# Kernel tuning notes

Measured on AMD Instinct MI355X. Metric: run time of the kernel, lower is better.

The kernel has to match this reference:

```python
import jax, jax.numpy as jnp
import numpy as np

BN_EPS = 1e-5

def gin_layer(x, src, dst, w1, b1, w2, b2, gamma, beta):
    # GINConv with eps=0: h_i = MLP(x_i + sum_{j->i} x_j)
    agg = jax.ops.segment_sum(x[src], dst, num_segments=x.shape[0])  # [N, D]
    h = x + agg
    h = jnp.maximum(h @ w1 + b1, 0.0) @ w2 + b2
    # BatchNorm (training-mode batch statistics, biased var as in torch)
    mu = jnp.mean(h, axis=0)
    var = jnp.var(h, axis=0)
    h = (h - mu) * jax.lax.rsqrt(var + BN_EPS) * gamma + beta
    return jnp.maximum(h, 0.0)  # ReLU (dropout = identity in eval)

def setup_inputs() -> dict:
    key = jax.random.key(0)
    N, E, G = 20000, 320000, 64
    dims = [128, 128, 256, 512]
    ks = jax.random.split(key, 32)
    inp = {
        "x": jax.random.normal(ks[0], (N, dims[0]), dtype=jnp.float32),
        "edge_index": jax.random.randint(ks[1], (2, E), 0, N, dtype=jnp.int64),
        "batch_idx": jnp.sort(jax.random.randint(ks[2], (N,), 0, G, dtype=jnp.int64)),
    }
    ki = 3
    for li, (di, do) in enumerate(zip(dims[:-1], dims[1:])):
        s = chr(ord('a') + li)
        inp[f"w1{s}"] = jax.random.normal(ks[ki], (di, do), dtype=jnp.float32) * (1.0 / np.sqrt(di)); ki += 1
        inp[f"b1{s}"] = jnp.zeros((do,), dtype=jnp.float32)
        inp[f"w2{s}"] = jax.random.normal(ks[ki], (do, do), dtype=jnp.float32) * (1.0 / np.sqrt(do)); ki += 1
        inp[f"b2{s}"] = jnp.zeros((do,), dtype=jnp.float32)
        inp[f"gn{s}"] = jnp.ones((do,), dtype=jnp.float32)
        inp[f"bn{s}"] = jnp.zeros((do,), dtype=jnp.float32)
    inp["wo"] = jax.random.normal(ks[ki], (dims[-1], 64), dtype=jnp.float32) * (1.0 / np.sqrt(dims[-1]))
    inp["bo"] = jnp.zeros((64,), dtype=jnp.float32)
    return inp

def reference(x, edge_index, batch_idx,
              w1a, b1a, w2a, b2a, gna, bna,
              w1b, b1b, w2b, b2b, gnb, bnb,
              w1c, b1c, w2c, b2c, gnc, bnc,
              wo, bo):
    G = 64
    src, dst = edge_index[0], edge_index[1]
    h = gin_layer(x, src, dst, w1a, b1a, w2a, b2a, gna, bna)
    h = gin_layer(h, src, dst, w1b, b1b, w2b, b2b, gnb, bnb)
    h = gin_layer(h, src, dst, w1c, b1c, w2c, b2c, gnc, bnc)
    # global mean pool over graphs
    sums = jax.ops.segment_sum(h, batch_idx, num_segments=G)  # [G, 512]
    cnts = jax.ops.segment_sum(jnp.ones((h.shape[0],), h.dtype), batch_idx, num_segments=G)
    pooled = sums / jnp.maximum(cnts, 1.0)[:, None]
    # output projection: Linear -> ReLU (dropout identity in eval)
    return jnp.maximum(pooled @ wo + bo, 0.0)
```

## Files before the change

### kernel.cpp

```cpp
#include <hip/hip_runtime.h>

typedef float f32x4 __attribute__((ext_vector_type(4)));
typedef _Float16 f16x2 __attribute__((ext_vector_type(2)));
typedef _Float16 f16x4 __attribute__((ext_vector_type(4)));
typedef _Float16 f16x8 __attribute__((ext_vector_type(8)));

__device__ __forceinline__ void gload_lds16(const _Float16* g, _Float16* l) {
  __builtin_amdgcn_global_load_lds(
      (const __attribute__((address_space(1))) unsigned int*)g,
      (__attribute__((address_space(3))) unsigned int*)l, 16, 0, 0);
}

__global__ __launch_bounds__(256) void hist_kernel(const int* __restrict__ dst,
                                                   int* __restrict__ deg, int E) {
  int e = blockIdx.x * 256 + threadIdx.x;
  if (e < E) atomicAdd(&deg[dst[e]], 1);
}

__global__ __launch_bounds__(1024) void scan_kernel(const int* __restrict__ deg,
                                                    int* __restrict__ rowstart,
                                                    int* __restrict__ cursor, int N) {
  __shared__ int sums[1024];
  const int t = threadIdx.x;
  const int CH = (N + 1023) >> 10;
  int local[32];
  int base = t * CH;
  int s = 0;
  for (int i = 0; i < CH; i++) {
    int idx = base + i;
    int v = (idx < N) ? deg[idx] : 0;
    local[i] = s;
    s += v;
  }
  sums[t] = s;
  __syncthreads();
  for (int off = 1; off < 1024; off <<= 1) {
    int add = (t >= off) ? sums[t - off] : 0;
    __syncthreads();
    sums[t] += add;
    __syncthreads();
  }
  int prefix = sums[t] - s;
  for (int i = 0; i < CH; i++) {
    int idx = base + i;
    if (idx < N) {
      int v = prefix + local[i];
      rowstart[idx] = v;
      cursor[idx] = v;
    }
  }
  if (t == 1023) rowstart[N] = sums[1023];
}

__global__ __launch_bounds__(256) void fill_kernel(const int* __restrict__ src,
                                                   const int* __restrict__ dst,
                                                   int* __restrict__ cursor,
                                                   int* __restrict__ nbr, int E) {
  int e = blockIdx.x * 256 + threadIdx.x;
  if (e >= E) return;
  int pos = atomicAdd(&cursor[dst[e]], 1);
  nbr[pos] = src[e];
}

__global__ __launch_bounds__(256) void xprep_kernel(const float4* __restrict__ in,
                                                    f16x4* __restrict__ out, int n4,
                                                    int* __restrict__ deg, int N,
                                                    float* __restrict__ zbuf, int zn) {
  int i = blockIdx.x * 256 + threadIdx.x;
  if (i < N) deg[i] = 0;
  if (i < zn) zbuf[i] = 0.f;
  if (i >= n4) return;
  float4 v = in[i];
  f16x4 h;
  h[0] = (_Float16)v.x; h[1] = (_Float16)v.y;
  h[2] = (_Float16)v.z; h[3] = (_Float16)v.w;
  out[i] = h;
}

template <int C, bool BNIN>
__global__ __launch_bounds__(256) void gather_agg_kernel(
    const _Float16* __restrict__ x, const int* __restrict__ rowstart,
    const int* __restrict__ nbr, const float* __restrict__ stats,
    const float* __restrict__ gamma, const float* __restrict__ beta,
    _Float16* __restrict__ agg, int N, float invN) {
  constexpr int Din = 64 * C;
  const int wave = threadIdx.x >> 6;
  const int lane = threadIdx.x & 63;
  const int node = blockIdx.x * 4 + wave;
  if (node >= N) return;

  float sc[C], sh[C];
  if constexpr (BNIN) {
#pragma unroll
    for (int j = 0; j < C; j++) {
      int c = lane * C + j;
      float mean = stats[c] * invN;
      float var = stats[Din + c] * invN - mean * mean;
      sc[j] = rsqrtf(var + 1e-5f) * gamma[c];
      sh[j] = beta[c] - mean * sc[j];
    }
  }

#define LOADROW(dstv, rowidx)                                              \
  {                                                                        \
    const _Float16* _p = x + (size_t)(rowidx)*Din + lane * C;              \
    if constexpr (C == 2) {                                                \
      f16x2 _t = *(const f16x2*)_p;                                        \
      dstv[0] = (float)_t[0]; dstv[1] = (float)_t[1];                      \
    } else {                                                               \
      f16x4 _t = *(const f16x4*)_p;                                        \
      dstv[0] = (float)_t[0]; dstv[1] = (float)_t[1];                      \
      dstv[2] = (float)_t[2]; dstv[3] = (float)_t[3];                      \
    }                                                                      \
  }
#define ACCUM(vv)                                                          \
  _Pragma("unroll") for (int j = 0; j < C; j++)                            \
      acc[j] += BNIN ? fmaxf(vv[j] * sc[j] + sh[j], 0.f) : vv[j];

  float acc[C];
  {
    float v[C];
    LOADROW(v, node)
#pragma unroll
    for (int j = 0; j < C; j++)
      acc[j] = BNIN ? fmaxf(v[j] * sc[j] + sh[j], 0.f) : v[j];
  }
  const int rs = rowstart[node], re = rowstart[node + 1];
  int e = rs;
  for (; e + 3 < re; e += 4) {
    int s0 = nbr[e], s1 = nbr[e + 1], s2 = nbr[e + 2], s3 = nbr[e + 3];
    float v0[C], v1[C], v2[C], v3[C];
    LOADROW(v0, s0)
    LOADROW(v1, s1)
    LOADROW(v2, s2)
    LOADROW(v3, s3)
    ACCUM(v0) ACCUM(v1) ACCUM(v2) ACCUM(v3)
  }
  for (; e + 1 < re; e += 2) {
    int s0 = nbr[e], s1 = nbr[e + 1];
    float v0[C], v1[C];
    LOADROW(v0, s0)
    LOADROW(v1, s1)
    ACCUM(v0) ACCUM(v1)
  }
  if (e < re) {
    int s0 = nbr[e];
    float v0[C];
    LOADROW(v0, s0)
    ACCUM(v0)
  }
#undef ACCUM
#undef LOADROW

  _Float16* o = agg + (size_t)node * Din + lane * C;
  if constexpr (C == 2) {
    f16x2 r; r[0] = (_Float16)acc[0]; r[1] = (_Float16)acc[1];
    *(f16x2*)o = r;
  } else {
    f16x4 r;
    r[0] = (_Float16)acc[0]; r[1] = (_Float16)acc[1];
    r[2] = (_Float16)acc[2]; r[3] = (_Float16)acc[3];
    *(f16x4*)o = r;
  }
}

struct WSeg {
  const float* W;
  _Float16* TH;
  int K, N, total;
};
struct WAll { WSeg s[6]; };

__global__ __launch_bounds__(256) void wprep_all_kernel(WAll a) {
  WSeg sg = a.s[blockIdx.y];
  int idx = blockIdx.x * 256 + threadIdx.x;
  if (idx >= sg.total) return;
  int k = idx / sg.N, n = idx - k * sg.N;
  int KT = sg.K >> 5;
  int frag = (n >> 4) * KT + (k >> 5);
  int slot = (n & 15) | (((k >> 3) & 3) << 4);
  sg.TH[(size_t)frag * 512 + slot * 8 + (k & 7)] = (_Float16)sg.W[idx];
}

template <int RT>
__global__ __launch_bounds__(256, 4) void gemm_mfma_kernel(
    const _Float16* __restrict__ A, const _Float16* __restrict__ BT,
    const float* __restrict__ bias, _Float16* __restrict__ Ch,
    int M, int K, int N, int mblocks, int cbShift,
    int doRelu, float* __restrict__ stats) {
  constexpr int NF = RT / 16;
  constexpr int NFT = 2 * NF;
  constexpr int FPW = NFT / 4;
  __shared__ _Float16 Ah[3][NFT * 512];
  const int bid = blockIdx.x;
  const int xcd = bid & 7;
  const int q = bid >> 3;
  const int r = ((q >> cbShift) << 3) + xcd;
  const int cb = q & ((1 << cbShift) - 1);
  if (r >= mblocks) return;

  const int tid = threadIdx.x;
  const int lane = tid & 63;
  const int w = tid >> 6;
  const int rowBase = r * RT;
  const int colBase = cb * 128 + w * 32;
  const int KT = K >> 5;

  f32x4 acc[NF][2] = {};
  const int c0 = colBase + (lane & 15);
  const size_t bBase0 = ((size_t)(colBase >> 4) * KT) * 512 + (size_t)lane * 8;
  const size_t bBase1 = bBase0 + (size_t)KT * 512;

  size_t srcOff[FPW];
#pragma unroll
  for (int i = 0; i < FPW; i++) {
    int F = w * FPW + i;
    int ks = F / NF, fi = F % NF;
    int row = rowBase + fi * 16 + (lane & 15);
    row = min(row, M - 1);
    srcOff[i] = (size_t)row * K + ks * 32 + ((lane >> 4) << 3);
  }

#define STAGE(b, t)                                                        \
  {                                                                        \
    _Pragma("unroll") for (int i = 0; i < FPW; i++)                        \
        gload_lds16(A + srcOff[i] + (size_t)(t) * 64,                      \
                    &Ah[b][(w * FPW + i) * 512]);                          \
  }

  const int NT = K >> 6;
  STAGE(0, 0)
  if (NT > 1) {
    STAGE(1, 1)
    if constexpr (FPW == 2)
      asm volatile("s_waitcnt vmcnt(2)" ::: "memory");
    else
      asm volatile("s_waitcnt vmcnt(1)" ::: "memory");
  } else {
    asm volatile("s_waitcnt vmcnt(0)" ::: "memory");
  }
  __builtin_amdgcn_s_barrier();
  __builtin_amdgcn_sched_barrier(0);

  int cur = 0;
  for (int t = 0; t < NT; t++) {
    f16x8 bh[2][2];
#pragma unroll
    for (int ks = 0; ks < 2; ks++) {
      int kf = t * 2 + ks;
      bh[ks][0] = *(const f16x8*)(BT + bBase0 + (size_t)kf * 512);
      bh[ks][1] = *(const f16x8*)(BT + bBase1 + (size_t)kf * 512);
    }
    __builtin_amdgcn_sched_barrier(0);
    if (t + 2 < NT) {
      int b2 = (cur >= 1) ? cur - 1 : 2;
      STAGE(b2, t + 2)
    }
    __builtin_amdgcn_sched_barrier(0);
#pragma unroll
    for (int ks = 0; ks < 2; ks++) {
#pragma unroll
      for (int fi = 0; fi < NF; fi++) {
        f16x8 ah = *(const f16x8*)(&Ah[cur][(ks * NF + fi) * 512 + lane * 8]);
        acc[fi][0] = __builtin_amdgcn_mfma_f32_16x16x32_f16(ah, bh[ks][0], acc[fi][0], 0, 0, 0);
        acc[fi][1] = __builtin_amdgcn_mfma_f32_16x16x32_f16(ah, bh[ks][1], acc[fi][1], 0, 0, 0);
      }
    }
    if (t + 1 < NT) {
      __builtin_amdgcn_s_barrier();
      __builtin_amdgcn_sched_barrier(0);
    }
    cur = (cur == 2) ? 0 : cur + 1;
  }
#undef STAGE

  const float bias0 = bias[c0], bias1 = bias[c0 + 16];
  float s1[2] = {0.f, 0.f}, s2[2] = {0.f, 0.f};
  const int rbase = rowBase + (lane >> 4) * 4;
#pragma unroll
  for (int fi = 0; fi < NF; fi++) {
#pragma unroll
    for (int j = 0; j < 4; j++) {
      int row = rbase + fi * 16 + j;
      float v0 = acc[fi][0][j] + bias0;
      float v1 = acc[fi][1][j] + bias1;
      if (doRelu) { v0 = fmaxf(v0, 0.f); v1 = fmaxf(v1, 0.f); }
      if (row < M) {
        Ch[(size_t)row * N + c0] = (_Float16)v0;
        Ch[(size_t)row * N + c0 + 16] = (_Float16)v1;
        s1[0] += v0; s2[0] += v0 * v0;
        s1[1] += v1; s2[1] += v1 * v1;
      }
    }
  }
  if (stats) {
#pragma unroll
    for (int off = 16; off < 64; off <<= 1) {
      s1[0] += __shfl_xor(s1[0], off);
      s2[0] += __shfl_xor(s2[0], off);
      s1[1] += __shfl_xor(s1[1], off);
      s2[1] += __shfl_xor(s2[1], off);
    }
    if (lane < 16) {
      atomicAdd(&stats[c0], s1[0]);
      atomicAdd(&stats[N + c0], s2[0]);
      atomicAdd(&stats[c0 + 16], s1[1]);
      atomicAdd(&stats[N + c0 + 16], s2[1]);
    }
  }
}

__global__ __launch_bounds__(256) void bn_pool_kernel(
    const _Float16* __restrict__ h, const float* __restrict__ stats,
    const float* __restrict__ gamma, const float* __restrict__ beta,
    const int* __restrict__ batch, float* __restrict__ pooled, int N, float invN) {
  const int g = blockIdx.x >> 3;
  const int s = blockIdx.x & 7;
  __shared__ int s_lo, s_hi;
  if (threadIdx.x == 0) {
    int lo = 0, hi = N;
    while (lo < hi) { int m = (lo + hi) >> 1; if (batch[m] < g) lo = m + 1; else hi = m; }
    s_lo = lo;
    lo = 0; hi = N;
    while (lo < hi) { int m = (lo + hi) >> 1; if (batch[m] < g + 1) lo = m + 1; else hi = m; }
    s_hi = lo;
  }
  __syncthreads();
  const int lo = s_lo, hi = s_hi, len = hi - lo;
  if (len == 0) return;
  const int per = (len + 7) >> 3;
  const int rs = lo + s * per;
  const int re = min(rs + per, hi);
  if (rs >= re) return;
  const int t = threadIdx.x;
  float scv[2], shv[2];
#pragma unroll
  for (int j = 0; j < 2; j++) {
    int c = 2 * t + j;
    float mean = stats[c] * invN;
    float var = stats[512 + c] * invN - mean * mean;
    scv[j] = rsqrtf(var + 1e-5f) * gamma[c];
    shv[j] = beta[c] - mean * scv[j];
  }
  float ax = 0.f, ay = 0.f;
  for (int r = rs; r < re; r++) {
    f16x2 v = *(const f16x2*)(h + (size_t)r * 512 + 2 * t);
    ax += fmaxf((float)v[0] * scv[0] + shv[0], 0.f);
    ay += fmaxf((float)v[1] * scv[1] + shv[1], 0.f);
  }
  float inv = 1.f / (float)len;
  atomicAdd(&pooled[g * 512 + 2 * t], ax * inv);
  atomicAdd(&pooled[g * 512 + 2 * t + 1], ay * inv);
}

__global__ __launch_bounds__(64) void out_kernel(const float* __restrict__ pooled,
                                                 const float* __restrict__ wo,
                                                 const float* __restrict__ bo,
                                                 float* __restrict__ out) {
  int g = blockIdx.x, o = threadIdx.x;
  float acc = bo[o];
  for (int c = 0; c < 512; c++) acc += pooled[g * 512 + c] * wo[c * 64 + o];
  out[g * 64 + o] = fmaxf(acc, 0.f);
}

extern "C" void kernel_launch(void* const* d_in, const int* in_sizes, int n_in,
                              void* d_out, int out_size, void* d_ws, size_t ws_size,
                              hipStream_t stream) {
  const float* x0 = (const float*)d_in[0];
  const int* ei = (const int*)d_in[1];
  const int* batch = (const int*)d_in[2];
  const int N = in_sizes[0] / 128;
  const int E = in_sizes[1] / 2;
  const int* src = ei;
  const int* dst = ei + E;
  const float* W[3][6];
  for (int li = 0; li < 3; li++)
    for (int k = 0; k < 6; k++) W[li][k] = (const float*)d_in[3 + li * 6 + k];
  const float* wo = (const float*)d_in[21];
  const float* bo = (const float*)d_in[22];
  float* out = (float*)d_out;

  float* stats3 = (float*)d_ws;
  float* pooled = stats3 + 3 * 1024;
  int* deg = (int*)(pooled + 64 * 512);
  int* rowstart = deg + N;
  int* cursor = rowstart + N + 1;
  int* nbr = cursor + N;
  uintptr_t wp = (uintptr_t)(nbr + E);
  wp = (wp + 15) & ~(uintptr_t)15;
  _Float16* aggh = (_Float16*)wp;
  _Float16* h1h = aggh + (size_t)N * 256;
  _Float16* h2h = h1h + (size_t)N * 512;
  _Float16* x0h = h2h + (size_t)N * 512;
  _Float16* wbuf = x0h + (size_t)N * 128;

  const int dins[3] = {128, 128, 256};
  const int douts[3] = {128, 256, 512};

  _Float16* WT[3][2];
  {
    _Float16* p = wbuf;
    for (int li = 0; li < 3; li++) {
      WT[li][0] = p; p += (size_t)dins[li] * douts[li];
      WT[li][1] = p; p += (size_t)douts[li] * douts[li];
    }
  }
  {
    WAll wa;
    int maxTotal = 0;
    for (int li = 0; li < 3; li++) {
      int e1 = dins[li] * douts[li];
      int e2 = douts[li] * douts[li];
      wa.s[li * 2 + 0] = WSeg{W[li][0], WT[li][0], dins[li], douts[li], e1};
      wa.s[li * 2 + 1] = WSeg{W[li][2], WT[li][1], douts[li], douts[li], e2};
      maxTotal = max(maxTotal, max(e1, e2));
    }
    dim3 g((maxTotal + 255) / 256, 6);
    wprep_all_kernel<<<g, 256, 0, stream>>>(wa);
  }

  {
    int n4 = N * 32;
    int zn = 3 * 1024 + 64 * 512;
    xprep_kernel<<<(n4 + 255) / 256, 256, 0, stream>>>(
        (const float4*)x0, (f16x4*)x0h, n4, deg, N, stats3, zn);
  }

  hist_kernel<<<(E + 255) / 256, 256, 0, stream>>>(dst, deg, E);
  scan_kernel<<<1, 1024, 0, stream>>>(deg, rowstart, cursor, N);
  fill_kernel<<<(E + 255) / 256, 256, 0, stream>>>(src, dst, cursor, nbr, E);

  const int mb64 = (N + 63) / 64;
  const int mb64_8 = ((mb64 + 7) / 8) * 8;
  const int mb32 = (N + 31) / 32;
  const int mb32_8 = ((mb32 + 7) / 8) * 8;
  const int gblocks = (N + 3) / 4;
  const float invN = 1.0f / N;

  for (int li = 0; li < 3; li++) {
    int Din = dins[li], Dout = douts[li];
    float* stats = stats3 + li * 1024;
    if (li == 0)
      gather_agg_kernel<2, false><<<gblocks, 256, 0, stream>>>(
          x0h, rowstart, nbr, nullptr, nullptr, nullptr, aggh, N, invN);
    else if (li == 1)
      gather_agg_kernel<2, true><<<gblocks, 256, 0, stream>>>(
          h2h, rowstart, nbr, stats3 + 0 * 1024, W[0][4], W[0][5], aggh, N, invN);
    else
      gather_agg_kernel<4, true><<<gblocks, 256, 0, stream>>>(
          h2h, rowstart, nbr, stats3 + 1 * 1024, W[1][4], W[1][5], aggh, N, invN);

    if (Dout == 128) {
      gemm_mfma_kernel<32><<<mb32_8, 256, 0, stream>>>(aggh, WT[li][0], W[li][1], h1h,
                                                       N, Din, Dout, mb32, 0, 1, nullptr);
      gemm_mfma_kernel<32><<<mb32_8, 256, 0, stream>>>(h1h, WT[li][1], W[li][3], h2h,
                                                       N, Dout, Dout, mb32, 0, 0, stats);
    } else {
      int cbShift = (Dout == 256) ? 1 : 2;
      int nblocks = mb64_8 << cbShift;
      gemm_mfma_kernel<64><<<nblocks, 256, 0, stream>>>(aggh, WT[li][0], W[li][1], h1h,
                                                        N, Din, Dout, mb64, cbShift, 1, nullptr);
      gemm_mfma_kernel<64><<<nblocks, 256, 0, stream>>>(h1h, WT[li][1], W[li][3], h2h,
                                                        N, Dout, Dout, mb64, cbShift, 0, stats);
    }
    if (li == 2) {
      bn_pool_kernel<<<64 * 8, 256, 0, stream>>>(
          h2h, stats3 + 2 * 1024, W[2][4], W[2][5], batch, pooled, N, invN);
    }
  }
  out_kernel<<<64, 64, 0, stream>>>(pooled, wo, bo, out);
}
```

Baseline: 266.6 us.

## Store GEMM A-operands in MFMA fragment-tiled layout for contiguous LDS staging

The gather kernel and the first GEMM of each layer now write their outputs directly in the 16x32 MFMA fragment-blocked layout used for weights. The following GEMM can then stage each A fragment with one contiguous 1 KB load instead of strided row loads, and the row clamping is dropped. Intermediate buffers are padded to a multiple of 64 rows to hold whole fragments. The cost is scattered 2-byte stores in the fragment epilogue and reads of uninitialized padding rows past N.

Result: no change. 266.5 us (-0.0%).

```diff
diff --git a/kernel.cpp b/kernel.cpp
--- a/kernel.cpp
+++ b/kernel.cpp
@@ -84,6 +84,7 @@
     const float* __restrict__ gamma, const float* __restrict__ beta,
     _Float16* __restrict__ agg, int N, float invN) {
   constexpr int Din = 64 * C;
+  constexpr int KT = Din >> 5;
   const int wave = threadIdx.x >> 6;
   const int lane = threadIdx.x & 63;
   const int node = blockIdx.x * 4 + wave;
@@ -152,15 +153,22 @@
 #undef ACCUM
 #undef LOADROW
 
-  _Float16* o = agg + (size_t)node * Din + lane * C;
+  int kt, lc, jj;
+  if constexpr (C == 4) {
+    kt = lane >> 3; lc = (lane >> 1) & 3; jj = (lane & 1) * 4;
+  } else {
+    kt = lane >> 4; lc = (lane >> 2) & 3; jj = (lane & 3) * 2;
+  }
+  size_t addr = (((size_t)(node >> 4) * KT + kt)) * 512 +
+                (size_t)((node & 15) | (lc << 4)) * 8 + jj;
   if constexpr (C == 2) {
     f16x2 r; r[0] = (_Float16)acc[0]; r[1] = (_Float16)acc[1];
-    *(f16x2*)o = r;
+    *(f16x2*)(agg + addr) = r;
   } else {
     f16x4 r;
     r[0] = (_Float16)acc[0]; r[1] = (_Float16)acc[1];
     r[2] = (_Float16)acc[2]; r[3] = (_Float16)acc[3];
-    *(f16x4*)o = r;
+    *(f16x4*)(agg + addr) = r;
   }
 }
 
@@ -182,7 +190,7 @@
   sg.TH[(size_t)frag * 512 + slot * 8 + (k & 7)] = (_Float16)sg.W[idx];
 }
 
-template <int RT>
+template <int RT, bool FRAGOUT>
 __global__ __launch_bounds__(256, 4) void gemm_mfma_kernel(
     const _Float16* __restrict__ A, const _Float16* __restrict__ BT,
     const float* __restrict__ bias, _Float16* __restrict__ Ch,
@@ -204,27 +212,25 @@
   const int w = tid >> 6;
   const int rowBase = r * RT;
   const int colBase = cb * 128 + w * 32;
-  const int KT = K >> 5;
+  const int KTa = K >> 5;
 
   f32x4 acc[NF][2] = {};
   const int c0 = colBase + (lane & 15);
-  const size_t bBase0 = ((size_t)(colBase >> 4) * KT) * 512 + (size_t)lane * 8;
-  const size_t bBase1 = bBase0 + (size_t)KT * 512;
+  const size_t bBase0 = ((size_t)(colBase >> 4) * KTa) * 512 + (size_t)lane * 8;
+  const size_t bBase1 = bBase0 + (size_t)KTa * 512;
 
   size_t srcOff[FPW];
 #pragma unroll
   for (int i = 0; i < FPW; i++) {
     int F = w * FPW + i;
     int ks = F / NF, fi = F % NF;
-    int row = rowBase + fi * 16 + (lane & 15);
-    row = min(row, M - 1);
-    srcOff[i] = (size_t)row * K + ks * 32 + ((lane >> 4) << 3);
+    srcOff[i] = (((size_t)((rowBase >> 4) + fi) * KTa) + ks) * 512 + (size_t)lane * 8;
   }
 
 #define STAGE(b, t)                                                        \
   {                                                                        \
     _Pragma("unroll") for (int i = 0; i < FPW; i++)                        \
-        gload_lds16(A + srcOff[i] + (size_t)(t) * 64,                      \
+        gload_lds16(A + srcOff[i] + (size_t)(t) * 1024,                    \
                     &Ah[b][(w * FPW + i) * 512]);                          \
   }
 
@@ -275,37 +281,58 @@
 #undef STAGE
 
   const float bias0 = bias[c0], bias1 = bias[c0 + 16];
-  float s1[2] = {0.f, 0.f}, s2[2] = {0.f, 0.f};
-  const int rbase = rowBase + (lane >> 4) * 4;
-#pragma unroll
-  for (int fi = 0; fi < NF; fi++) {
-#pragma unroll
-    for (int j = 0; j < 4; j++) {
-      int row = rbase + fi * 16 + j;
-      float v0 = acc[fi][0][j] + bias0;
-      float v1 = acc[fi][1][j] + bias1;
-      if (doRelu) { v0 = fmaxf(v0, 0.f); v1 = fmaxf(v1, 0.f); }
-      if (row < M) {
-        Ch[(size_t)row * N + c0] = (_Float16)v0;
-        Ch[(size_t)row * N + c0 + 16] = (_Float16)v1;
-        s1[0] += v0; s2[0] += v0 * v0;
-        s1[1] += v1; s2[1] += v1 * v1;
+  if constexpr (FRAGOUT) {
+    const int KTo = N >> 5;
+    const int row16b = (lane >> 4) * 4;
+    const int e0 = (lane & 15) & 7;
+    const int lc0 = ((lane & 15) >> 3);
+    const int kfo = (colBase >> 5);
+#pragma unroll
+    for (int fi = 0; fi < NF; fi++) {
+      size_t fragRow = (size_t)((rowBase >> 4) + ((rowBase & 16) ? 0 : 0) + fi);
+      size_t base = ((size_t)((rowBase >> 4) + fi) * KTo + kfo) * 512;
+#pragma unroll
+      for (int j = 0; j < 4; j++) {
+        int slotRow = row16b + j;
+        float v0 = fmaxf(acc[fi][0][j] + bias0, 0.f);
+        float v1 = fmaxf(acc[fi][1][j] + bias1, 0.f);
+        Ch[base + (size_t)(slotRow | (lc0 << 4)) * 8 + e0] = (_Float16)v0;
+        Ch[base + (size_t)(slotRow | ((lc0 + 2) << 4)) * 8 + e0] = (_Float16)v1;
       }
     }
-  }
-  if (stats) {
-#pragma unroll
-    for (int off = 16; off < 64; off <<= 1) {
-      s1[0] += __shfl_xor(s1[0], off);
-      s2[0] += __shfl_xor(s2[0], off);
-      s1[1] += __shfl_xor(s1[1], off);
-      s2[1] += __shfl_xor(s2[1], off);
-    }
-    if (lane < 16) {
-      atomicAdd(&stats[c0], s1[0]);
-      atomicAdd(&stats[N + c0], s2[0]);
-      atomicAdd(&stats[c0 + 16], s1[1]);
-      atomicAdd(&stats[N + c0 + 16], s2[1]);
+  } else {
+    float s1[2] = {0.f, 0.f}, s2[2] = {0.f, 0.f};
+    const int rbase = rowBase + (lane >> 4) * 4;
+#pragma unroll
+    for (int fi = 0; fi < NF; fi++) {
+#pragma unroll
+      for (int j = 0; j < 4; j++) {
+        int row = rbase + fi * 16 + j;
+        float v0 = acc[fi][0][j] + bias0;
+        float v1 = acc[fi][1][j] + bias1;
+        if (doRelu) { v0 = fmaxf(v0, 0.f); v1 = fmaxf(v1, 0.f); }
+        if (row < M) {
+          Ch[(size_t)row * N + c0] = (_Float16)v0;
+          Ch[(size_t)row * N + c0 + 16] = (_Float16)v1;
+          s1[0] += v0; s2[0] += v0 * v0;
+          s1[1] += v1; s2[1] += v1 * v1;
+        }
+      }
+    }
+    if (stats) {
+#pragma unroll
+      for (int off = 16; off < 64; off <<= 1) {
+        s1[0] += __shfl_xor(s1[0], off);
+        s2[0] += __shfl_xor(s2[0], off);
+        s1[1] += __shfl_xor(s1[1], off);
+        s2[1] += __shfl_xor(s2[1], off);
+      }
+      if (lane < 16) {
+        atomicAdd(&stats[c0], s1[0]);
+        atomicAdd(&stats[N + c0], s2[0]);
+        atomicAdd(&stats[c0 + 16], s1[1]);
+        atomicAdd(&stats[N + c0 + 16], s2[1]);
+      }
     }
   }
 }
@@ -380,6 +407,9 @@
   const float* bo = (const float*)d_in[22];
   float* out = (float*)d_out;
 
+  const int mb64 = (N + 63) / 64;
+  const int NP = mb64 * 64;
+
   float* stats3 = (float*)d_ws;
   float* pooled = stats3 + 3 * 1024;
   int* deg = (int*)(pooled + 64 * 512);
@@ -389,8 +419,8 @@
   uintptr_t wp = (uintptr_t)(nbr + E);
   wp = (wp + 15) & ~(uintptr_t)15;
   _Float16* aggh = (_Float16*)wp;
-  _Float16* h1h = aggh + (size_t)N * 256;
-  _Float16* h2h = h1h + (size_t)N * 512;
+  _Float16* h1h = aggh + (size_t)NP * 256;
+  _Float16* h2h = h1h + (size_t)NP * 512;
   _Float16* x0h = h2h + (size_t)N * 512;
   _Float16* wbuf = x0h + (size_t)N * 128;
 
@@ -430,7 +460,6 @@
   scan_kernel<<<1, 1024, 0, stream>>>(deg, rowstart, cursor, N);
   fill_kernel<<<(E + 255) / 256, 256, 0, stream>>>(src, dst, cursor, nbr, E);
 
-  const int mb64 = (N + 63) / 64;
   const int mb64_8 = ((mb64 + 7) / 8) * 8;
   const int mb32 = (N + 31) / 32;
   const int mb32_8 = ((mb32 + 7) / 8) * 8;
@@ -451,17 +480,17 @@
           h2h, rowstart, nbr, stats3 + 1 * 1024, W[1][4], W[1][5], aggh, N, invN);
 
     if (Dout == 128) {
-      gemm_mfma_kernel<32><<<mb32_8, 256, 0, stream>>>(aggh, WT[li][0], W[li][1], h1h,
-                                                       N, Din, Dout, mb32, 0, 1, nullptr);
-      gemm_mfma_kernel<32><<<mb32_8, 256, 0, stream>>>(h1h, WT[li][1], W[li][3], h2h,
-                                                       N, Dout, Dout, mb32, 0, 0, stats);
+      gemm_mfma_kernel<32, true><<<mb32_8, 256, 0, stream>>>(aggh, WT[li][0], W[li][1], h1h,
+                                                             N, Din, Dout, mb32, 0, 1, nullptr);
+      gemm_mfma_kernel<32, false><<<mb32_8, 256, 0, stream>>>(h1h, WT[li][1], W[li][3], h2h,
+                                                              N, Dout, Dout, mb32, 0, 0, stats);
     } else {
       int cbShift = (Dout == 256) ? 1 : 2;
       int nblocks = mb64_8 << cbShift;
-      gemm_mfma_kernel<64><<<nblocks, 256, 0, stream>>>(aggh, WT[li][0], W[li][1], h1h,
-                                                        N, Din, Dout, mb64, cbShift, 1, nullptr);
-      gemm_mfma_kernel<64><<<nblocks, 256, 0, stream>>>(h1h, WT[li][1], W[li][3], h2h,
-                                                        N, Dout, Dout, mb64, cbShift, 0, stats);
+      gemm_mfma_kernel<64, true><<<nblocks, 256, 0, stream>>>(aggh, WT[li][0], W[li][1], h1h,
+                                                              N, Din, Dout, mb64, cbShift, 1, nullptr);
+      gemm_mfma_kernel<64, false><<<nblocks, 256, 0, stream>>>(h1h, WT[li][1], W[li][3], h2h,
+                                                               N, Dout, Dout, mb64, cbShift, 0, stats);
     }
     if (li == 2) {
       bn_pool_kernel<<<64 * 8, 256, 0, stream>>>(
```
